# Kernel optimization log

Hardware: AMD Instinct MI355X
Metric: run time of the kernel (lower is better)

Reference implementation:

```python
import jax, jax.numpy as jnp
import numpy as np

H = W = 512                      # image_size=512 hardcoded in nr.Renderer
VIEW_TAN = float(np.tan(30.0 * np.pi / 180.0))  # nr default viewing angle
NEAR = 0.1
BIG = 1e10
CHUNK = 64                       # faces per scan step


def setup_inputs() -> dict:
    key = jax.random.key(0)
    k1, k2, k3, k4 = jax.random.split(key, 4)
    V, F = 2048, 4096
    v = jax.random.normal(k1, (1, V, 3), dtype=jnp.float32)
    # __init__ normalization: center and scale to unit cube
    v_max = v.max(axis=1, keepdims=True)
    v_min = v.min(axis=1, keepdims=True)
    v = (v - (v_max + v_min) / 2.0) / ((v_max - v_min).max() / 2.0)
    faces = jax.random.randint(k2, (1, F, 3), 0, V, dtype=jnp.int32)
    textures = jax.random.uniform(k3, (1, F, 2, 2, 2, 3), dtype=jnp.float32)
    image_ref = jax.random.uniform(k4, (1, 3, H, W), dtype=jnp.float32)
    camera_position = jnp.array([0.0, 0.0, -2.732], dtype=jnp.float32)
    camera_up = jnp.array([0.0, 1.0, 0.0], dtype=jnp.float32)
    return {"vertices": v, "faces": faces, "textures": textures,
            "camera_position": camera_position, "camera_up": camera_up,
            "image_ref": image_ref}


def _normalize(x):
    return x / (jnp.linalg.norm(x) + 1e-12)


def _render(vertices, faces, textures, camera_position, camera_up):
    # --- look_at camera transform (at = origin) ---
    eye = camera_position
    z_axis = _normalize(-eye)                       # forward
    x_axis = _normalize(jnp.cross(_normalize(camera_up), z_axis))
    y_axis = jnp.cross(z_axis, x_axis)
    R = jnp.stack([x_axis, y_axis, z_axis], axis=0)  # rows
    v_cam = (vertices[0] - eye) @ R.T               # [V,3]
    # --- perspective projection to NDC ---
    zc = v_cam[:, 2]
    proj = v_cam[:, :2] / (zc[:, None] * VIEW_TAN + 1e-12)  # [V,2]

    # per-face constant label colors (textures are tiled base colors)
    cols = textures[0].mean(axis=(1, 2, 3))          # [F,3]
    tri_xy = proj[faces[0]]                          # [F,3,2]
    tri_z = zc[faces[0]]                             # [F,3]

    # pixel centers in NDC, row 0 at top (y=+1)
    xs = (jnp.arange(W, dtype=jnp.float32) + 0.5) * 2.0 / W - 1.0
    ys = 1.0 - (jnp.arange(H, dtype=jnp.float32) + 0.5) * 2.0 / H
    xx, yy = jnp.meshgrid(xs, ys)                    # [H,W]
    pix = jnp.stack([xx, yy], axis=-1).reshape(-1, 2)  # [P,2]
    P = pix.shape[0]

    F = tri_xy.shape[0]
    S = F // CHUNK
    chunks = (tri_xy.reshape(S, CHUNK, 3, 2),
              tri_z.reshape(S, CHUNK, 3),
              cols.reshape(S, CHUNK, 3))

    def cross2(a, b):
        return a[..., 0] * b[..., 1] - a[..., 1] * b[..., 0]

    def step(carry, chunk):
        zbuf, color = carry                          # [P], [P,3]
        txy, tz, tc = chunk
        p0, p1, p2 = txy[:, 0], txy[:, 1], txy[:, 2]  # [C,2]
        area = cross2(p1 - p0, p2 - p0)              # [C]
        safe_area = jnp.where(jnp.abs(area) > 1e-8, area, 1.0)
        d = pix[:, None, :]                          # [P,1,2]
        w0 = cross2(p2 - p1, d - p1)                 # [P,C]
        w1 = cross2(p0 - p2, d - p2)
        w2 = cross2(p1 - p0, d - p0)
        s = jnp.sign(area)
        inside = ((w0 * s >= 0) & (w1 * s >= 0) & (w2 * s >= 0)
                  & (jnp.abs(area) > 1e-8))          # [P,C]
        b0, b1, b2 = w0 / safe_area, w1 / safe_area, w2 / safe_area
        z = b0 * tz[:, 0] + b1 * tz[:, 1] + b2 * tz[:, 2]  # [P,C]
        zm = jnp.where(inside & (z > NEAR), z, BIG)
        j = jnp.argmin(zm, axis=1)                   # [P]
        zmin = jnp.take_along_axis(zm, j[:, None], axis=1)[:, 0]
        col = tc[j]                                  # [P,3]
        upd = zmin < zbuf
        zbuf = jnp.where(upd, zmin, zbuf)
        color = jnp.where(upd[:, None], col, color)
        return (zbuf, color), None

    init = (jnp.full((P,), BIG, dtype=jnp.float32),
            jnp.zeros((P, 3), dtype=jnp.float32))
    (zbuf, color), _ = jax.lax.scan(step, init, chunks)
    image = color.reshape(H, W, 3).transpose(2, 0, 1)[None]  # [1,3,H,W]
    return image


def reference(vertices, faces, textures, camera_position, camera_up, image_ref):
    image = _render(vertices, faces, textures, camera_position, camera_up)
    image = image[:, ::-1]  # .flip(dims=[1]) -> channel flip as in source
    loss = jnp.sum((image - image_ref) ** 2)
    return loss
```

## Files before the change

### kernel.cpp

```cpp
#include <hip/hip_runtime.h>

#define IMG_H 512
#define IMG_W 512
#define VIEW_TAN_F 0.57735026918962576451f
#define NEARZ 0.1f
#define BIGF 1e10f

#define TILE 32
#define NTX (IMG_W / TILE)
#define NTILES (NTX * NTX)
#define RSPLITS 32
#define RCHUNK 256


__global__ void prep_faces(const float* __restrict__ verts,
                           const int* __restrict__ faces,
                           const float* __restrict__ tex,
                           const float* __restrict__ campos,
                           const float* __restrict__ camup,
                           float4* __restrict__ fd,
                           float* __restrict__ cols,
                           unsigned long long* __restrict__ zbuf,
                           int F)
{
    int gid = blockIdx.x * blockDim.x + threadIdx.x;

    if (zbuf) {
        const int P = IMG_H * IMG_W;
        for (int i = gid; i < P; i += gridDim.x * blockDim.x)
            zbuf[i] = ~0ull;
    }

    int f = gid;
    if (f >= F) return;

    float ex = campos[0], ey = campos[1], ez = campos[2];
    float ux = camup[0], uy = camup[1], uz = camup[2];
    float zxv = -ex, zyv = -ey, zzv = -ez;
    float inv = 1.0f / (sqrtf(zxv*zxv + zyv*zyv + zzv*zzv) + 1e-12f);
    zxv *= inv; zyv *= inv; zzv *= inv;
    inv = 1.0f / (sqrtf(ux*ux + uy*uy + uz*uz) + 1e-12f);
    ux *= inv; uy *= inv; uz *= inv;
    float xxv = uy*zzv - uz*zyv;
    float xyv = uz*zxv - ux*zzv;
    float xzv = ux*zyv - uy*zxv;
    inv = 1.0f / (sqrtf(xxv*xxv + xyv*xyv + xzv*xzv) + 1e-12f);
    xxv *= inv; xyv *= inv; xzv *= inv;
    float yxv = zyv*xzv - zzv*xyv;
    float yyv = zzv*xxv - zxv*xzv;
    float yzv = zxv*xyv - zyv*xxv;

    float px_[3], py_[3], pz_[3];
    #pragma unroll
    for (int k = 0; k < 3; ++k) {
        int vi = faces[f*3 + k];
        float vx = verts[vi*3+0] - ex;
        float vy = verts[vi*3+1] - ey;
        float vz = verts[vi*3+2] - ez;
        float cx = xxv*vx + xyv*vy + xzv*vz;
        float cy = yxv*vx + yyv*vy + yzv*vz;
        float cz = zxv*vx + zyv*vy + zzv*vz;
        float denom = cz * VIEW_TAN_F + 1e-12f;
        px_[k] = cx / denom;
        py_[k] = cy / denom;
        pz_[k] = cz;
    }
    float x0 = px_[0], y0 = py_[0];
    float x1 = px_[1], y1 = py_[1];
    float x2 = px_[2], y2 = py_[2];
    float area = (x1-x0)*(y2-y0) - (y1-y0)*(x2-x0);
    bool valid = fabsf(area) > 1e-8f;
    float safe = valid ? area : 1.0f;
    float s = (area > 0.0f) ? 1.0f : -1.0f;

    float A0 = -(y2-y1), B0 = (x2-x1), C0 = (y2-y1)*x1 - (x2-x1)*y1;
    float A1 = -(y0-y2), B1 = (x0-x2), C1 = (y0-y2)*x2 - (x0-x2)*y2;
    float A2 = -(y1-y0), B2 = (x1-x0), C2 = (y1-y0)*x0 - (x1-x0)*y0;

    float invs = 1.0f / safe;
    float Az = (A0*pz_[0] + A1*pz_[1] + A2*pz_[2]) * invs;
    float Bz = (B0*pz_[0] + B1*pz_[1] + B2*pz_[2]) * invs;
    float Cz = (C0*pz_[0] + C1*pz_[1] + C2*pz_[2]) * invs;

    A0 *= s; B0 *= s; C0 *= s;
    A1 *= s; B1 *= s; C1 *= s;
    A2 *= s; B2 *= s; C2 *= s;

    if (!valid) {
        A0 = B0 = A1 = B1 = A2 = B2 = 0.0f;
        C0 = C1 = C2 = -1.0f;
        Az = Bz = 0.0f; Cz = 0.0f;
    }

    fd[f*3+0] = make_float4(A0, B0, C0, A1);
    fd[f*3+1] = make_float4(B1, C1, A2, B2);
    fd[f*3+2] = make_float4(C2, Az, Bz, Cz);

    float c0 = 0.0f, c1 = 0.0f, c2 = 0.0f;
    #pragma unroll
    for (int t = 0; t < 8; ++t) {
        c0 += tex[f*24 + t*3 + 0];
        c1 += tex[f*24 + t*3 + 1];
        c2 += tex[f*24 + t*3 + 2];
    }
    cols[f*3+0] = c0 * 0.125f;
    cols[f*3+1] = c1 * 0.125f;
    cols[f*3+2] = c2 * 0.125f;
}

__global__ __launch_bounds__(256) void bin_tiles(
    const float4* __restrict__ fd, int F,
    int* __restrict__ counts, int* __restrict__ lists)
{
    __shared__ int sCnt;
    int tile = blockIdx.x;
    int tX = tile & (NTX - 1);
    int tY = tile >> 4;
    int tid  = threadIdx.x;
    int lane = tid & 63;

    float cx = ((float)(tX * TILE + TILE/2)) * (2.0f / IMG_W) - 1.0f;
    float cy = 1.0f - ((float)(tY * TILE + TILE/2)) * (2.0f / IMG_H);
    const float hx = (TILE/2) * (2.0f / IMG_W);
    const float hy = (TILE/2) * (2.0f / IMG_H);

    if (tid == 0) sCnt = 0;
    __syncthreads();

    int* mylist = lists + (size_t)tile * F;
    for (int c0f = 0; c0f < F; c0f += 256) {
        int f = c0f + tid;
        bool pass = false;
        if (f < F) {
            float4 q0 = fd[3*f + 0];
            float4 q1 = fd[3*f + 1];
            float4 q2 = fd[3*f + 2];
            float e0 = fmaf(q0.x, cx, fmaf(q0.y, cy, q0.z)) + fabsf(q0.x)*hx + fabsf(q0.y)*hy;
            float e1 = fmaf(q0.w, cx, fmaf(q1.x, cy, q1.y)) + fabsf(q0.w)*hx + fabsf(q1.x)*hy;
            float e2 = fmaf(q1.z, cx, fmaf(q1.w, cy, q2.x)) + fabsf(q1.z)*hx + fabsf(q1.w)*hy;
            pass = fminf(fminf(e0, e1), e2) >= -1e-6f;
        }
        unsigned long long m = __ballot(pass);
        int wbase = 0;
        if (lane == 0 && m) wbase = atomicAdd(&sCnt, __popcll(m));
        wbase = __shfl(wbase, 0, 64);
        if (pass) {
            int pos = wbase + __popcll(m & ((1ull << lane) - 1ull));
            mylist[pos] = f;
        }
    }
    __syncthreads();
    if (tid == 0) counts[tile] = sCnt;
}

__global__ __launch_bounds__(256) void raster_binned(
    const float4* __restrict__ fd,
    const int* __restrict__ counts, const int* __restrict__ lists, int F,
    unsigned long long* __restrict__ zbuf)
{
    __shared__ float4 sA[RCHUNK][3];
    __shared__ int    sFi[RCHUNK];

    int b     = blockIdx.x;
    int split = b & (RSPLITS - 1);
    int tile  = b >> 5;
    int n = counts[tile];
    int total_j = (n > split) ? ((n - split + RSPLITS - 1) / RSPLITS) : 0;
    if (total_j == 0) return;

    int tX = tile & (NTX - 1);
    int tY = tile >> 4;
    int tid = threadIdx.x;

    int colp = tX * TILE + (tid & 31);
    int row0 = tY * TILE + (tid >> 5);
    float x  = ((float)colp + 0.5f) * (2.0f / IMG_W) - 1.0f;
    float y0 = 1.0f - ((float)row0 + 0.5f) * (2.0f / IMG_H);

    float bz[4] = {BIGF, BIGF, BIGF, BIGF};
    int   bi[4] = {-1, -1, -1, -1};

    const int* mylist = lists + (size_t)tile * F;

    for (int j0 = 0; j0 < total_j; j0 += RCHUNK) {
        int m = min(RCHUNK, total_j - j0);
        __syncthreads();
        if (tid < m) {
            int e  = split + RSPLITS * (j0 + tid);
            int fi = mylist[e];
            sFi[tid]  = fi;
            sA[tid][0] = fd[3*fi + 0];
            sA[tid][1] = fd[3*fi + 1];
            sA[tid][2] = fd[3*fi + 2];
        }
        __syncthreads();

        for (int s = 0; s < m; ++s) {
            float4 p0 = sA[s][0], p1 = sA[s][1], p2 = sA[s][2];
            int fi = sFi[s];
            float w0x = fmaf(p0.x, x, p0.z);
            float w1x = fmaf(p0.w, x, p1.y);
            float w2x = fmaf(p1.z, x, p2.x);
            float zx  = fmaf(p2.y, x, p2.w);
            #pragma unroll
            for (int k = 0; k < 4; ++k) {
                float yk = y0 - (float)k * 0.03125f;
                float w0 = fmaf(p0.y, yk, w0x);
                float w1 = fmaf(p1.x, yk, w1x);
                float w2 = fmaf(p1.w, yk, w2x);
                float z  = fmaf(p2.z, yk, zx);
                bool hit = (fminf(fminf(w0, w1), w2) >= 0.0f) && (z > NEARZ);
                if (hit && z < bz[k]) { bz[k] = z; bi[k] = fi; }
            }
        }
    }

    #pragma unroll
    for (int k = 0; k < 4; ++k) {
        if (bi[k] >= 0) {
            int p = (row0 + 8*k) * IMG_W + colp;
            unsigned long long key =
                ((unsigned long long)__float_as_uint(bz[k]) << 32) | (unsigned)bi[k];
            atomicMin(&zbuf[p], key);
        }
    }
}

__global__ __launch_bounds__(256) void resolve_loss(
    const unsigned long long* __restrict__ zbuf,
    const float* __restrict__ cols,
    const float* __restrict__ imref,
    float* __restrict__ out)
{
    int p = blockIdx.x * 256 + threadIdx.x;
    unsigned long long key = zbuf[p];
    unsigned idx = (unsigned)(key & 0xffffffffull);
    float r = 0.0f, g = 0.0f, bl = 0.0f;
    if (idx != 0xffffffffu) {
        r  = cols[idx*3 + 0];
        g  = cols[idx*3 + 1];
        bl = cols[idx*3 + 2];
    }
    const int HW = IMG_H * IMG_W;
    float d0 = bl - imref[0*HW + p];
    float d1 = g  - imref[1*HW + p];
    float d2 = r  - imref[2*HW + p];
    float loss = fmaf(d0, d0, fmaf(d1, d1, d2*d2));

    #pragma unroll
    for (int off = 32; off > 0; off >>= 1)
        loss += __shfl_down(loss, off, 64);

    __shared__ float wsum[4];
    int wid  = threadIdx.x >> 6;
    int lane = threadIdx.x & 63;
    if (lane == 0) wsum[wid] = loss;
    __syncthreads();
    if (threadIdx.x == 0)
        atomicAdd(out, wsum[0] + wsum[1] + wsum[2] + wsum[3]);
}

__global__ __launch_bounds__(256) void raster_loss_mono(
    const float4* __restrict__ fd,
    const float* __restrict__ cols,
    const float* __restrict__ imref,
    float* __restrict__ out, int F)
{
    int p = blockIdx.x * 256 + threadIdx.x;
    int col = p & (IMG_W - 1);
    float x = ((float)col + 0.5f) * (2.0f / IMG_W) - 1.0f;
    float y = 1.0f - ((float)(p >> 9) + 0.5f) * (2.0f / IMG_H);

    float bestz = BIGF;
    int besti = -1;
    for (int f = 0; f < F; ++f) {
        float4 q0 = fd[3*f + 0];
        float4 q1 = fd[3*f + 1];
        float4 q2 = fd[3*f + 2];
        float w0 = fmaf(q0.x, x, fmaf(q0.y, y, q0.z));
        float w1 = fmaf(q0.w, x, fmaf(q1.x, y, q1.y));
        float w2 = fmaf(q1.z, x, fmaf(q1.w, y, q2.x));
        float z  = fmaf(q2.y, x, fmaf(q2.z, y, q2.w));
        bool hit = (w0 >= 0.0f) & (w1 >= 0.0f) & (w2 >= 0.0f) & (z > NEARZ);
        float zm = hit ? z : BIGF;
        if (zm < bestz) { bestz = zm; besti = f; }
    }
    float r = 0.0f, g = 0.0f, bl = 0.0f;
    if (besti >= 0) { r = cols[besti*3]; g = cols[besti*3+1]; bl = cols[besti*3+2]; }
    const int HW = IMG_H * IMG_W;
    float d0 = bl - imref[p], d1 = g - imref[HW+p], d2 = r - imref[2*HW+p];
    float loss = fmaf(d0, d0, fmaf(d1, d1, d2*d2));
    #pragma unroll
    for (int off = 32; off > 0; off >>= 1)
        loss += __shfl_down(loss, off, 64);
    __shared__ float wsum[4];
    int wid = threadIdx.x >> 6, lane = threadIdx.x & 63;
    if (lane == 0) wsum[wid] = loss;
    __syncthreads();
    if (threadIdx.x == 0)
        atomicAdd(out, wsum[0] + wsum[1] + wsum[2] + wsum[3]);
}

extern "C" void kernel_launch(void* const* d_in, const int* in_sizes, int n_in,
                              void* d_out, int out_size, void* d_ws, size_t ws_size,
                              hipStream_t stream)
{
    const float* verts  = (const float*)d_in[0];
    const int*   faces  = (const int*)d_in[1];
    const float* tex    = (const float*)d_in[2];
    const float* campos = (const float*)d_in[3];
    const float* camup  = (const float*)d_in[4];
    const float* imref  = (const float*)d_in[5];
    int F = in_sizes[1] / 3;

    const int P = IMG_H * IMG_W;
    size_t zbytes  = (size_t)P * 8;
    size_t cntB    = (size_t)NTILES * 4;
    size_t listB   = (size_t)NTILES * F * 4;
    size_t fdbytes = (size_t)F * 3 * sizeof(float4);
    size_t cbytes  = (size_t)F * 3 * sizeof(float);
    float* out = (float*)d_out;

    hipMemsetAsync(d_out, 0, sizeof(float), stream);

    if (ws_size >= zbytes + cntB + listB + fdbytes + cbytes) {
        char* w = (char*)d_ws;
        unsigned long long* zbuf = (unsigned long long*)w;          w += zbytes;
        int*    cnts = (int*)w;                                     w += cntB;
        int*    lst  = (int*)w;                                     w += listB;
        float4* fd   = (float4*)w;                                  w += fdbytes;
        float*  cols = (float*)w;

        int pgrid = (F + 255)/256 > 64 ? (F + 255)/256 : 64;
        prep_faces<<<pgrid, 256, 0, stream>>>(verts, faces, tex, campos, camup, fd, cols, zbuf, F);
        bin_tiles<<<NTILES, 256, 0, stream>>>(fd, F, cnts, lst);
        raster_binned<<<NTILES * RSPLITS, 256, 0, stream>>>(fd, cnts, lst, F, zbuf);
        resolve_loss<<<P/256, 256, 0, stream>>>(zbuf, cols, imref, out);
    } else {
        float4* fd   = (float4*)d_ws;
        float*  cols = (float*)((char*)d_ws + fdbytes);
        prep_faces<<<(F + 255)/256, 256, 0, stream>>>(verts, faces, tex, campos, camup, fd, cols,
                                                      (unsigned long long*)nullptr, F);
        raster_loss_mono<<<P/256, 256, 0, stream>>>(fd, cols, imref, out, F);
    }
}
```

Measured before the change: 119.8 us.

## Fuse face prep with per-face bbox binning into 16x16 tiles

Removes the separate per-tile binning kernel, which tested every face against every tile. Instead, each face thread walks only the tiles its screen bounding box overlaps and appends itself to their lists with global atomics. Tiles shrink from 32x32 to 16x16 with fewer splits per tile, so each raster thread handles one pixel. The output memset is folded into the prep kernel. The costs are global atomic contention on the tile counters, a nondeterministic order of faces within each list, and an extra memset for the counters.

```diff
diff --git a/kernel.cpp b/kernel.cpp
--- a/kernel.cpp
+++ b/kernel.cpp
@@ -6,24 +6,29 @@
 #define NEARZ 0.1f
 #define BIGF 1e10f
 
-#define TILE 32
+#define TILE 16
 #define NTX (IMG_W / TILE)
 #define NTILES (NTX * NTX)
-#define RSPLITS 32
+#define RSPLITS 8
 #define RCHUNK 256
 
 
-__global__ void prep_faces(const float* __restrict__ verts,
-                           const int* __restrict__ faces,
-                           const float* __restrict__ tex,
-                           const float* __restrict__ campos,
-                           const float* __restrict__ camup,
-                           float4* __restrict__ fd,
-                           float* __restrict__ cols,
-                           unsigned long long* __restrict__ zbuf,
-                           int F)
+__global__ void prep_bin(const float* __restrict__ verts,
+                         const int* __restrict__ faces,
+                         const float* __restrict__ tex,
+                         const float* __restrict__ campos,
+                         const float* __restrict__ camup,
+                         float4* __restrict__ fd,
+                         float* __restrict__ cols,
+                         unsigned long long* __restrict__ zbuf,
+                         int* __restrict__ counts,
+                         int* __restrict__ lists,
+                         float* __restrict__ out,
+                         int F)
 {
     int gid = blockIdx.x * blockDim.x + threadIdx.x;
+
+    if (gid == 0 && out) out[0] = 0.0f;
 
     if (zbuf) {
         const int P = IMG_H * IMG_W;
@@ -106,51 +111,45 @@
     cols[f*3+0] = c0 * 0.125f;
     cols[f*3+1] = c1 * 0.125f;
     cols[f*3+2] = c2 * 0.125f;
-}
-
-__global__ __launch_bounds__(256) void bin_tiles(
-    const float4* __restrict__ fd, int F,
-    int* __restrict__ counts, int* __restrict__ lists)
-{
-    __shared__ int sCnt;
-    int tile = blockIdx.x;
-    int tX = tile & (NTX - 1);
-    int tY = tile >> 4;
-    int tid  = threadIdx.x;
-    int lane = tid & 63;
-
-    float cx = ((float)(tX * TILE + TILE/2)) * (2.0f / IMG_W) - 1.0f;
-    float cy = 1.0f - ((float)(tY * TILE + TILE/2)) * (2.0f / IMG_H);
+
+    if (!valid || !lists) return;
+
+    float sxmin = fminf(fminf(x0, x1), x2);
+    float sxmax = fmaxf(fmaxf(x0, x1), x2);
+    float symin = fminf(fminf(y0, y1), y2);
+    float symax = fmaxf(fmaxf(y0, y1), y2);
+
+    int c0p = (int)ceilf ((sxmin + 1.0f) * 256.0f - 0.5f) - 1;
+    int c1p = (int)floorf((sxmax + 1.0f) * 256.0f - 0.5f) + 1;
+    int r0p = (int)ceilf ((1.0f - symax) * 256.0f - 0.5f) - 1;
+    int r1p = (int)floorf((1.0f - symin) * 256.0f - 0.5f) + 1;
+    c0p = max(c0p, 0); c1p = min(c1p, IMG_W - 1);
+    r0p = max(r0p, 0); r1p = min(r1p, IMG_H - 1);
+    if (c0p > c1p || r0p > r1p) return;
+
+    int tx0 = c0p / TILE, tx1 = c1p / TILE;
+    int ty0 = r0p / TILE, ty1 = r1p / TILE;
+
     const float hx = (TILE/2) * (2.0f / IMG_W);
     const float hy = (TILE/2) * (2.0f / IMG_H);
-
-    if (tid == 0) sCnt = 0;
-    __syncthreads();
-
-    int* mylist = lists + (size_t)tile * F;
-    for (int c0f = 0; c0f < F; c0f += 256) {
-        int f = c0f + tid;
-        bool pass = false;
-        if (f < F) {
-            float4 q0 = fd[3*f + 0];
-            float4 q1 = fd[3*f + 1];
-            float4 q2 = fd[3*f + 2];
-            float e0 = fmaf(q0.x, cx, fmaf(q0.y, cy, q0.z)) + fabsf(q0.x)*hx + fabsf(q0.y)*hy;
-            float e1 = fmaf(q0.w, cx, fmaf(q1.x, cy, q1.y)) + fabsf(q0.w)*hx + fabsf(q1.x)*hy;
-            float e2 = fmaf(q1.z, cx, fmaf(q1.w, cy, q2.x)) + fabsf(q1.z)*hx + fabsf(q1.w)*hy;
-            pass = fminf(fminf(e0, e1), e2) >= -1e-6f;
+    float d0 = fabsf(A0)*hx + fabsf(B0)*hy;
+    float d1 = fabsf(A1)*hx + fabsf(B1)*hy;
+    float d2 = fabsf(A2)*hx + fabsf(B2)*hy;
+
+    for (int ty = ty0; ty <= ty1; ++ty) {
+        float cy = 1.0f - ((float)(ty * TILE + TILE/2)) * (2.0f / IMG_H);
+        for (int tx = tx0; tx <= tx1; ++tx) {
+            float cx = ((float)(tx * TILE + TILE/2)) * (2.0f / IMG_W) - 1.0f;
+            float e0 = fmaf(A0, cx, fmaf(B0, cy, C0)) + d0;
+            float e1 = fmaf(A1, cx, fmaf(B1, cy, C1)) + d1;
+            float e2 = fmaf(A2, cx, fmaf(B2, cy, C2)) + d2;
+            if (fminf(fminf(e0, e1), e2) >= -1e-6f) {
+                int tile = ty * NTX + tx;
+                int pos = atomicAdd(&counts[tile], 1);
+                lists[(size_t)tile * F + pos] = f;
+            }
         }
-        unsigned long long m = __ballot(pass);
-        int wbase = 0;
-        if (lane == 0 && m) wbase = atomicAdd(&sCnt, __popcll(m));
-        wbase = __shfl(wbase, 0, 64);
-        if (pass) {
-            int pos = wbase + __popcll(m & ((1ull << lane) - 1ull));
-            mylist[pos] = f;
-        }
-    }
-    __syncthreads();
-    if (tid == 0) counts[tile] = sCnt;
+    }
 }
 
 __global__ __launch_bounds__(256) void raster_binned(
@@ -163,22 +162,22 @@
 
     int b     = blockIdx.x;
     int split = b & (RSPLITS - 1);
-    int tile  = b >> 5;
+    int tile  = b >> 3;
     int n = counts[tile];
     int total_j = (n > split) ? ((n - split + RSPLITS - 1) / RSPLITS) : 0;
     if (total_j == 0) return;
 
     int tX = tile & (NTX - 1);
-    int tY = tile >> 4;
+    int tY = tile >> 5;
     int tid = threadIdx.x;
 
-    int colp = tX * TILE + (tid & 31);
-    int row0 = tY * TILE + (tid >> 5);
-    float x  = ((float)colp + 0.5f) * (2.0f / IMG_W) - 1.0f;
-    float y0 = 1.0f - ((float)row0 + 0.5f) * (2.0f / IMG_H);
-
-    float bz[4] = {BIGF, BIGF, BIGF, BIGF};
-    int   bi[4] = {-1, -1, -1, -1};
+    int colp = tX * TILE + (tid & 15);
+    int rowp = tY * TILE + (tid >> 4);
+    float x = ((float)colp + 0.5f) * (2.0f / IMG_W) - 1.0f;
+    float y = 1.0f - ((float)rowp + 0.5f) * (2.0f / IMG_H);
+
+    float bz = BIGF;
+    int   bi = -1;
 
     const int* mylist = lists + (size_t)tile * F;
 
@@ -188,7 +187,7 @@
         if (tid < m) {
             int e  = split + RSPLITS * (j0 + tid);
             int fi = mylist[e];
-            sFi[tid]  = fi;
+            sFi[tid]   = fi;
             sA[tid][0] = fd[3*fi + 0];
             sA[tid][1] = fd[3*fi + 1];
             sA[tid][2] = fd[3*fi + 2];
@@ -198,31 +197,20 @@
         for (int s = 0; s < m; ++s) {
             float4 p0 = sA[s][0], p1 = sA[s][1], p2 = sA[s][2];
             int fi = sFi[s];
-            float w0x = fmaf(p0.x, x, p0.z);
-            float w1x = fmaf(p0.w, x, p1.y);
-            float w2x = fmaf(p1.z, x, p2.x);
-            float zx  = fmaf(p2.y, x, p2.w);
-            #pragma unroll
-            for (int k = 0; k < 4; ++k) {
-                float yk = y0 - (float)k * 0.03125f;
-                float w0 = fmaf(p0.y, yk, w0x);
-                float w1 = fmaf(p1.x, yk, w1x);
-                float w2 = fmaf(p1.w, yk, w2x);
-                float z  = fmaf(p2.z, yk, zx);
-                bool hit = (fminf(fminf(w0, w1), w2) >= 0.0f) && (z > NEARZ);
-                if (hit && z < bz[k]) { bz[k] = z; bi[k] = fi; }
-            }
+            float w0 = fmaf(p0.x, x, fmaf(p0.y, y, p0.z));
+            float w1 = fmaf(p0.w, x, fmaf(p1.x, y, p1.y));
+            float w2 = fmaf(p1.z, x, fmaf(p1.w, y, p2.x));
+            float z  = fmaf(p2.y, x, fmaf(p2.z, y, p2.w));
+            bool hit = (fminf(fminf(w0, w1), w2) >= 0.0f) && (z > NEARZ);
+            if (hit && z < bz) { bz = z; bi = fi; }
         }
     }
 
-    #pragma unroll
-    for (int k = 0; k < 4; ++k) {
-        if (bi[k] >= 0) {
-            int p = (row0 + 8*k) * IMG_W + colp;
-            unsigned long long key =
-                ((unsigned long long)__float_as_uint(bz[k]) << 32) | (unsigned)bi[k];
-            atomicMin(&zbuf[p], key);
-        }
+    if (bi >= 0) {
+        int p = rowp * IMG_W + colp;
+        unsigned long long key =
+            ((unsigned long long)__float_as_uint(bz) << 32) | (unsigned)bi;
+        atomicMin(&zbuf[p], key);
     }
 }
 
@@ -321,8 +309,6 @@
     size_t cbytes  = (size_t)F * 3 * sizeof(float);
     float* out = (float*)d_out;
 
-    hipMemsetAsync(d_out, 0, sizeof(float), stream);
-
     if (ws_size >= zbytes + cntB + listB + fdbytes + cbytes) {
         char* w = (char*)d_ws;
         unsigned long long* zbuf = (unsigned long long*)w;          w += zbytes;
@@ -331,16 +317,20 @@
         float4* fd   = (float4*)w;                                  w += fdbytes;
         float*  cols = (float*)w;
 
+        hipMemsetAsync(cnts, 0, cntB, stream);
         int pgrid = (F + 255)/256 > 64 ? (F + 255)/256 : 64;
-        prep_faces<<<pgrid, 256, 0, stream>>>(verts, faces, tex, campos, camup, fd, cols, zbuf, F);
-        bin_tiles<<<NTILES, 256, 0, stream>>>(fd, F, cnts, lst);
+        prep_bin<<<pgrid, 256, 0, stream>>>(verts, faces, tex, campos, camup,
+                                            fd, cols, zbuf, cnts, lst, out, F);
         raster_binned<<<NTILES * RSPLITS, 256, 0, stream>>>(fd, cnts, lst, F, zbuf);
         resolve_loss<<<P/256, 256, 0, stream>>>(zbuf, cols, imref, out);
     } else {
         float4* fd   = (float4*)d_ws;
         float*  cols = (float*)((char*)d_ws + fdbytes);
-        prep_faces<<<(F + 255)/256, 256, 0, stream>>>(verts, faces, tex, campos, camup, fd, cols,
-                                                      (unsigned long long*)nullptr, F);
+        hipMemsetAsync(d_out, 0, sizeof(float), stream);
+        prep_bin<<<(F + 255)/256, 256, 0, stream>>>(verts, faces, tex, campos, camup,
+                                                    fd, cols, (unsigned long long*)nullptr,
+                                                    (int*)nullptr, (int*)nullptr,
+                                                    (float*)nullptr, F);
         raster_loss_mono<<<P/256, 256, 0, stream>>>(fd, cols, imref, out, F);
     }
 }
```

Result: slower. 228.4 us (+90.6%).

## Shrink raster tiles to 16x16 with fewer splits and fold output zeroing into prep

Applied to the files above, without the earlier changes.

Changes screen tiles from 32x32 to 16x16 (1024 tiles) and cuts per-tile face splits from 32 to 8, so each raster thread handles one pixel instead of four. Smaller tiles give tighter binning and fewer faces tested per pixel. The price is four times as many bin_tiles blocks and a lists buffer four times larger. Separately, it drops the hipMemsetAsync for the loss output, zeroing it inside prep_faces instead, and raises the prep grid floor.

```diff
diff --git a/kernel.cpp b/kernel.cpp
--- a/kernel.cpp
+++ b/kernel.cpp
@@ -6,10 +6,10 @@
 #define NEARZ 0.1f
 #define BIGF 1e10f
 
-#define TILE 32
+#define TILE 16
 #define NTX (IMG_W / TILE)
 #define NTILES (NTX * NTX)
-#define RSPLITS 32
+#define RSPLITS 8
 #define RCHUNK 256
 
 
@@ -21,9 +21,12 @@
                            float4* __restrict__ fd,
                            float* __restrict__ cols,
                            unsigned long long* __restrict__ zbuf,
+                           float* __restrict__ out,
                            int F)
 {
     int gid = blockIdx.x * blockDim.x + threadIdx.x;
+
+    if (gid == 0 && out) out[0] = 0.0f;
 
     if (zbuf) {
         const int P = IMG_H * IMG_W;
@@ -115,7 +118,7 @@
     __shared__ int sCnt;
     int tile = blockIdx.x;
     int tX = tile & (NTX - 1);
-    int tY = tile >> 4;
+    int tY = tile >> 5;
     int tid  = threadIdx.x;
     int lane = tid & 63;
 
@@ -163,22 +166,22 @@
 
     int b     = blockIdx.x;
     int split = b & (RSPLITS - 1);
-    int tile  = b >> 5;
+    int tile  = b >> 3;
     int n = counts[tile];
     int total_j = (n > split) ? ((n - split + RSPLITS - 1) / RSPLITS) : 0;
     if (total_j == 0) return;
 
     int tX = tile & (NTX - 1);
-    int tY = tile >> 4;
+    int tY = tile >> 5;
     int tid = threadIdx.x;
 
-    int colp = tX * TILE + (tid & 31);
-    int row0 = tY * TILE + (tid >> 5);
-    float x  = ((float)colp + 0.5f) * (2.0f / IMG_W) - 1.0f;
-    float y0 = 1.0f - ((float)row0 + 0.5f) * (2.0f / IMG_H);
-
-    float bz[4] = {BIGF, BIGF, BIGF, BIGF};
-    int   bi[4] = {-1, -1, -1, -1};
+    int colp = tX * TILE + (tid & 15);
+    int rowp = tY * TILE + (tid >> 4);
+    float x = ((float)colp + 0.5f) * (2.0f / IMG_W) - 1.0f;
+    float y = 1.0f - ((float)rowp + 0.5f) * (2.0f / IMG_H);
+
+    float bz = BIGF;
+    int   bi = -1;
 
     const int* mylist = lists + (size_t)tile * F;
 
@@ -188,7 +191,7 @@
         if (tid < m) {
             int e  = split + RSPLITS * (j0 + tid);
             int fi = mylist[e];
-            sFi[tid]  = fi;
+            sFi[tid]   = fi;
             sA[tid][0] = fd[3*fi + 0];
             sA[tid][1] = fd[3*fi + 1];
             sA[tid][2] = fd[3*fi + 2];
@@ -198,31 +201,20 @@
         for (int s = 0; s < m; ++s) {
             float4 p0 = sA[s][0], p1 = sA[s][1], p2 = sA[s][2];
             int fi = sFi[s];
-            float w0x = fmaf(p0.x, x, p0.z);
-            float w1x = fmaf(p0.w, x, p1.y);
-            float w2x = fmaf(p1.z, x, p2.x);
-            float zx  = fmaf(p2.y, x, p2.w);
-            #pragma unroll
-            for (int k = 0; k < 4; ++k) {
-                float yk = y0 - (float)k * 0.03125f;
-                float w0 = fmaf(p0.y, yk, w0x);
-                float w1 = fmaf(p1.x, yk, w1x);
-                float w2 = fmaf(p1.w, yk, w2x);
-                float z  = fmaf(p2.z, yk, zx);
-                bool hit = (fminf(fminf(w0, w1), w2) >= 0.0f) && (z > NEARZ);
-                if (hit && z < bz[k]) { bz[k] = z; bi[k] = fi; }
-            }
+            float w0 = fmaf(p0.x, x, fmaf(p0.y, y, p0.z));
+            float w1 = fmaf(p0.w, x, fmaf(p1.x, y, p1.y));
+            float w2 = fmaf(p1.z, x, fmaf(p1.w, y, p2.x));
+            float z  = fmaf(p2.y, x, fmaf(p2.z, y, p2.w));
+            bool hit = (fminf(fminf(w0, w1), w2) >= 0.0f) && (z > NEARZ);
+            if (hit && z < bz) { bz = z; bi = fi; }
         }
     }
 
-    #pragma unroll
-    for (int k = 0; k < 4; ++k) {
-        if (bi[k] >= 0) {
-            int p = (row0 + 8*k) * IMG_W + colp;
-            unsigned long long key =
-                ((unsigned long long)__float_as_uint(bz[k]) << 32) | (unsigned)bi[k];
-            atomicMin(&zbuf[p], key);
-        }
+    if (bi >= 0) {
+        int p = rowp * IMG_W + colp;
+        unsigned long long key =
+            ((unsigned long long)__float_as_uint(bz) << 32) | (unsigned)bi;
+        atomicMin(&zbuf[p], key);
     }
 }
 
@@ -321,8 +313,6 @@
     size_t cbytes  = (size_t)F * 3 * sizeof(float);
     float* out = (float*)d_out;
 
-    hipMemsetAsync(d_out, 0, sizeof(float), stream);
-
     if (ws_size >= zbytes + cntB + listB + fdbytes + cbytes) {
         char* w = (char*)d_ws;
         unsigned long long* zbuf = (unsigned long long*)w;          w += zbytes;
@@ -331,16 +321,19 @@
         float4* fd   = (float4*)w;                                  w += fdbytes;
         float*  cols = (float*)w;
 
-        int pgrid = (F + 255)/256 > 64 ? (F + 255)/256 : 64;
-        prep_faces<<<pgrid, 256, 0, stream>>>(verts, faces, tex, campos, camup, fd, cols, zbuf, F);
+        int pgrid = (F + 255)/256 > 128 ? (F + 255)/256 : 128;
+        prep_faces<<<pgrid, 256, 0, stream>>>(verts, faces, tex, campos, camup,
+                                              fd, cols, zbuf, out, F);
         bin_tiles<<<NTILES, 256, 0, stream>>>(fd, F, cnts, lst);
         raster_binned<<<NTILES * RSPLITS, 256, 0, stream>>>(fd, cnts, lst, F, zbuf);
         resolve_loss<<<P/256, 256, 0, stream>>>(zbuf, cols, imref, out);
     } else {
         float4* fd   = (float4*)d_ws;
         float*  cols = (float*)((char*)d_ws + fdbytes);
-        prep_faces<<<(F + 255)/256, 256, 0, stream>>>(verts, faces, tex, campos, camup, fd, cols,
-                                                      (unsigned long long*)nullptr, F);
+        hipMemsetAsync(d_out, 0, sizeof(float), stream);
+        prep_faces<<<(F + 255)/256, 256, 0, stream>>>(verts, faces, tex, campos, camup,
+                                                      fd, cols, (unsigned long long*)nullptr,
+                                                      (float*)nullptr, F);
         raster_loss_mono<<<P/256, 256, 0, stream>>>(fd, cols, imref, out, F);
     }
 }
```

Result: slower. 126.4 us (+5.5%).
